# Kernel tuning notes

Hardware: AMD Instinct MI355X
Metric: run time of the kernel (lower is better)

The kernel has to match this reference:

```python
import jax, jax.numpy as jnp
import numpy as np

EPS = 1e-12

def _l2norm(x):
    return x / jnp.maximum(jnp.linalg.norm(x, axis=-1, keepdims=True), EPS)

def setup_inputs() -> dict:
    key = jax.random.key(0)
    ks = jax.random.split(key, 11)
    B, L, HID, M = 64, 512, 768, 128
    R, P, T = 64, 8, 32
    return {
        "hidden_states": jax.random.normal(ks[0], (B, L, HID), dtype=jnp.float32),
        "ctx_mask": jax.random.randint(ks[1], (B, L), 0, 2, dtype=jnp.int32),
        "between_mask": jax.random.randint(ks[2], (B, L), 0, 2, dtype=jnp.int32),
        "subj_type_id": jax.random.randint(ks[3], (B,), 0, T, dtype=jnp.int32),
        "obj_type_id": jax.random.randint(ks[4], (B,), 0, T, dtype=jnp.int32),
        "subj_first": jax.random.randint(ks[5], (B,), 0, 2, dtype=jnp.int32),
        "proj_W": jax.random.normal(ks[6], (HID, M), dtype=jnp.float32) * 0.02,
        "label_probes": jax.random.normal(ks[7], (R, P, M), dtype=jnp.float32) * 0.02,
        "subj_type_W": jax.random.normal(ks[8], (T, M), dtype=jnp.float32) * 0.02,
        "obj_type_W": jax.random.normal(ks[9], (T, M), dtype=jnp.float32) * 0.02,
        "dir_W": jax.random.normal(ks[10], (2, M), dtype=jnp.float32) * 0.02,
    }

def reference(hidden_states, ctx_mask, between_mask, subj_type_id, obj_type_id,
              subj_first, proj_W, label_probes, subj_type_W, obj_type_W, dir_W):
    # Document token embeddings: project + L2 normalize. [B, L, M]
    D = _l2norm(hidden_states @ proj_W)

    between = between_mask.astype(bool)
    ctx = ctx_mask.astype(bool)
    has_between = jnp.any(between, axis=1)  # [B]
    evidence = jnp.where(has_between[:, None], between, ctx)  # [B, L]

    # Conditioned probes: [B, R, P, M]
    Q = (label_probes[None]
         + subj_type_W[subj_type_id][:, None, None]
         + obj_type_W[obj_type_id][:, None, None]
         + dir_W[subj_first][:, None, None])
    Q = _l2norm(Q)

    # MaxSim: [B, R, P, L]
    sim = jnp.einsum('brhm,blm->brhl', Q, D)
    sim = jnp.where(evidence[:, None, None, :], sim, -10000.0)
    mx = sim.max(axis=3)                        # [B, R, P]
    mx = jnp.where(mx > -1000.0, mx, 0.0)       # zero out fully-masked probes
    logits = mx.sum(axis=2)                     # [B, R]
    return logits
```

## Files before the change

kernel.cpp:

```cpp
#include <hip/hip_runtime.h>
#include <hip/hip_bf16.h>

typedef __attribute__((ext_vector_type(8))) __bf16 bf16x8;
typedef __attribute__((ext_vector_type(4))) float f32x4;

#define B_   64
#define L_   512
#define HID_ 768
#define M_   128
#define R_   64
#define P_   8

__device__ __forceinline__ int swz(int row, int k, int stride) {
    return row * stride + (k ^ ((row & 7) << 3));
}
__device__ __forceinline__ int swz4(int row, int k) {
    return row * 128 + (k ^ ((row & 15) << 3));
}

#define GLL16(gp, lp)                                                        \
    __builtin_amdgcn_global_load_lds(                                        \
        (const __attribute__((address_space(1))) void*)(gp),                 \
        (__attribute__((address_space(3))) void*)(lp), 16, 0, 0)

__device__ __forceinline__ bf16x8 cvt8(float4 f0, float4 f1) {
    bf16x8 v;
    v[0]=(__bf16)f0.x; v[1]=(__bf16)f0.y; v[2]=(__bf16)f0.z; v[3]=(__bf16)f0.w;
    v[4]=(__bf16)f1.x; v[5]=(__bf16)f1.y; v[6]=(__bf16)f1.z; v[7]=(__bf16)f1.w;
    return v;
}

__global__ __launch_bounds__(256) void k_wt(const float* __restrict__ W,
                                            __bf16* __restrict__ Wt) {
    int idx = blockIdx.x * 256 + threadIdx.x;
    int k = idx >> 7, n = idx & 127;
    int c = k >> 6, kk = k & 63;
    Wt[c * 8192 + n * 64 + (kk ^ ((n & 7) << 3))] = (__bf16)W[idx];
}

__global__ __launch_bounds__(512, 4) void k_proj(const float* __restrict__ hidden,
                                                 const __bf16* __restrict__ Wt,
                                                 __bf16* __restrict__ D) {
    __shared__ __align__(16) float  Alf[2][64 * 64];
    __shared__ __align__(16) __bf16 Bl[2][128 * 64];
    __shared__ float nbuf[2][64];
    const int t = threadIdx.x;
    const int lane = t & 63, w = t >> 6;
    const int rlo = lane & 15, g = lane >> 4;
    const int rb = w & 3, ch = w >> 2;
    const int row0 = blockIdx.x * 512 + blockIdx.y * 64;

    f32x4 acc[4] = {};

    const int sr0 = t >> 4;
    const int scg = t & 15;
    const float* hbase = hidden + (size_t)row0 * HID_;

#define STAGE_A(ci_, buf_)                                                     \
    {                                                                          \
        _Pragma("unroll")                                                      \
        for (int h = 0; h < 2; ++h) {                                          \
            const int row = h * 32 + sr0;                                      \
            const int cgs = scg ^ (row & 7);                                   \
            GLL16(hbase + (size_t)row * HID_ + (ci_) * 64 + cgs * 4,           \
                  &Alf[buf_][(h * 8 + w) * 256 + lane * 4]);                   \
        }                                                                      \
    }
#define STAGE_B(ci_, buf_)                                                     \
    {                                                                          \
        const __bf16* wsrc = Wt + (ci_) * 8192 + w * 1024;                     \
        GLL16(wsrc + lane * 8,       &Bl[buf_][w * 1024]);                     \
        GLL16(wsrc + 512 + lane * 8, &Bl[buf_][w * 1024 + 512]);               \
    }

    STAGE_A(0, 0);
    STAGE_B(0, 0);

    for (int ci = 0; ci < 12; ++ci) {
        const int cur = ci & 1;
        if (ci < 11) {
            STAGE_A(ci + 1, cur ^ 1);
            STAGE_B(ci + 1, cur ^ 1);
            asm volatile("s_waitcnt vmcnt(4)" ::: "memory");
        } else {
            asm volatile("s_waitcnt vmcnt(0)" ::: "memory");
        }
        __builtin_amdgcn_sched_barrier(0);
        __builtin_amdgcn_s_barrier();

#pragma unroll
        for (int s = 0; s < 2; ++s) {
            const int row = rb * 16 + rlo;
            const int kkg = s * 8 + g * 2;
            const int x = row & 7;
            float4 a0 = *(const float4*)&Alf[cur][row * 64 + ((kkg ^ x) * 4)];
            float4 a1 = *(const float4*)&Alf[cur][row * 64 + (((kkg + 1) ^ x) * 4)];
            bf16x8 aF = cvt8(a0, a1);
            const int kk = s * 32 + g * 8;
#pragma unroll
            for (int c = 0; c < 4; ++c) {
                bf16x8 bF = *(const bf16x8*)&Bl[cur][swz(ch * 64 + c * 16 + rlo, kk, 64)];
                acc[c] = __builtin_amdgcn_mfma_f32_16x16x32_bf16(aF, bF, acc[c], 0, 0, 0);
            }
        }
        __builtin_amdgcn_s_barrier();
    }
#undef STAGE_A
#undef STAGE_B

    float ss[4] = {0.f, 0.f, 0.f, 0.f};
#pragma unroll
    for (int c = 0; c < 4; ++c)
#pragma unroll
        for (int r = 0; r < 4; ++r) ss[r] += acc[c][r] * acc[c][r];
#pragma unroll
    for (int r = 0; r < 4; ++r)
#pragma unroll
        for (int off = 1; off < 16; off <<= 1) ss[r] += __shfl_xor(ss[r], off);
    if (rlo == 0) {
#pragma unroll
        for (int r = 0; r < 4; ++r) nbuf[ch][rb * 16 + g * 4 + r] = ss[r];
    }
    __syncthreads();
    float sc[4];
#pragma unroll
    for (int r = 0; r < 4; ++r) {
        float tot = nbuf[0][rb * 16 + g * 4 + r] + nbuf[1][rb * 16 + g * 4 + r];
        sc[r] = 1.0f / fmaxf(sqrtf(tot), 1e-12f);
    }

    __bf16* Dst = (__bf16*)Alf;
#pragma unroll
    for (int c = 0; c < 4; ++c)
#pragma unroll
        for (int r = 0; r < 4; ++r) {
            int row = rb * 16 + g * 4 + r;
            int col = ch * 64 + c * 16 + rlo;
            Dst[swz4(row, col)] = (__bf16)(acc[c][r] * sc[r]);
        }
    __syncthreads();
#pragma unroll
    for (int h = 0; h < 2; ++h) {
        int row = (t >> 4) + h * 32;
        int seg = t & 15;
        bf16x8 v = *(const bf16x8*)&Dst[row * 128 + seg * 8];
        *(bf16x8*)(D + (size_t)(row0 + row) * M_ + seg * 8) = v;
    }
}

__global__ __launch_bounds__(256) void k_sim(const float* __restrict__ lp,
                                             const float* __restrict__ sW,
                                             const float* __restrict__ oW,
                                             const float* __restrict__ dW,
                                             const int* __restrict__ st,
                                             const int* __restrict__ ot,
                                             const int* __restrict__ sf,
                                             const int* __restrict__ ctx,
                                             const int* __restrict__ btw,
                                             const __bf16* __restrict__ D,
                                             float* __restrict__ out) {
    __shared__ __align__(16) __bf16 Dl[2][128 * 128];
    __shared__ float evl[L_];
    __shared__ int anyf;
    const int t = threadIdx.x;
    const int lane = t & 63, w = t >> 6;
    const int rlo = lane & 15, g = lane >> 4;
    const int b = blockIdx.x, pt = blockIdx.y;

    const __bf16* Db = D + (size_t)b * L_ * M_;

#pragma unroll
    for (int q = 0; q < 8; ++q)
        GLL16(Db + q * 2048 + w * 512 + lane * 8, &Dl[0][q * 2048 + w * 512]);

    if (t == 0) anyf = 0;
    __syncthreads();
    int v0 = btw[b * L_ + t], v1 = btw[b * L_ + t + 256];
    int c0 = ctx[b * L_ + t], c1 = ctx[b * L_ + t + 256];
    if (v0 | v1) anyf = 1;
    __syncthreads();
    const int any = anyf;
    evl[t]       = (any ? v0 : c0) ? 1.0f : 0.0f;
    evl[t + 256] = (any ? v1 : c1) ? 1.0f : 0.0f;

    const int sb = st[b], ob = ot[b], db = sf[b];
    const float* sv = sW + sb * M_;
    const float* ov = oW + ob * M_;
    const float* dv = dW + db * M_;
    bf16x8 qF[2][4];
#pragma unroll
    for (int pt2 = 0; pt2 < 2; ++pt2) {
        const float* lpp = lp + (size_t)(pt * 128 + w * 32 + pt2 * 16 + rlo) * M_;
        float qv[32];
        float ssq = 0.f;
#pragma unroll
        for (int ks = 0; ks < 4; ++ks) {
#pragma unroll
            for (int h = 0; h < 2; ++h) {
                const int m0 = ks * 32 + g * 8 + h * 4;
                float4 a  = *(const float4*)(lpp + m0);
                float4 s4 = *(const float4*)(sv + m0);
                float4 o4 = *(const float4*)(ov + m0);
                float4 d4 = *(const float4*)(dv + m0);
                float x0 = a.x + s4.x + o4.x + d4.x;
                float x1 = a.y + s4.y + o4.y + d4.y;
                float x2 = a.z + s4.z + o4.z + d4.z;
                float x3 = a.w + s4.w + o4.w + d4.w;
                qv[ks * 8 + h * 4 + 0] = x0;
                qv[ks * 8 + h * 4 + 1] = x1;
                qv[ks * 8 + h * 4 + 2] = x2;
                qv[ks * 8 + h * 4 + 3] = x3;
                ssq += x0 * x0 + x1 * x1 + x2 * x2 + x3 * x3;
            }
        }
        ssq += __shfl_xor(ssq, 16);
        ssq += __shfl_xor(ssq, 32);
        const float scq = 1.0f / fmaxf(sqrtf(ssq), 1e-12f);
#pragma unroll
        for (int ks = 0; ks < 4; ++ks)
#pragma unroll
            for (int j = 0; j < 8; ++j)
                qF[pt2][ks][j] = (__bf16)(qv[ks * 8 + j] * scq);
    }

    __syncthreads();

    float vmax[2][4];
#pragma unroll
    for (int pt2 = 0; pt2 < 2; ++pt2)
#pragma unroll
        for (int r = 0; r < 4; ++r) vmax[pt2][r] = -1e30f;

    for (int tc = 0; tc < 4; ++tc) {
        const int cur = tc & 1;
        if (tc < 3) {
#pragma unroll
            for (int q = 0; q < 8; ++q)
                GLL16(Db + (tc + 1) * 16384 + q * 2048 + w * 512 + lane * 8,
                      &Dl[cur ^ 1][q * 2048 + w * 512]);
        }
#pragma unroll
        for (int tt = 0; tt < 8; ++tt) {
            f32x4 pacc[2] = {};
#pragma unroll
            for (int ks = 0; ks < 4; ++ks) {
                bf16x8 bF = *(const bf16x8*)&Dl[cur][swz4(tt * 16 + rlo, ks * 32 + g * 8)];
                pacc[0] = __builtin_amdgcn_mfma_f32_16x16x32_bf16(qF[0][ks], bF, pacc[0], 0, 0, 0);
                pacc[1] = __builtin_amdgcn_mfma_f32_16x16x32_bf16(qF[1][ks], bF, pacc[1], 0, 0, 0);
            }
            const float e = evl[tc * 128 + tt * 16 + rlo];
#pragma unroll
            for (int pt2 = 0; pt2 < 2; ++pt2)
#pragma unroll
                for (int r = 0; r < 4; ++r) {
                    float sv2 = (e > 0.5f) ? pacc[pt2][r] : -1e4f;
                    vmax[pt2][r] = fmaxf(vmax[pt2][r], sv2);
                }
        }
        __syncthreads();
    }

#pragma unroll
    for (int pt2 = 0; pt2 < 2; ++pt2)
#pragma unroll
        for (int r = 0; r < 4; ++r)
#pragma unroll
            for (int off = 1; off < 16; off <<= 1)
                vmax[pt2][r] = fmaxf(vmax[pt2][r], __shfl_xor(vmax[pt2][r], off));

#pragma unroll
    for (int pt2 = 0; pt2 < 2; ++pt2) {
        float psum = 0.f;
#pragma unroll
        for (int r = 0; r < 4; ++r)
            psum += (vmax[pt2][r] > -1000.0f) ? vmax[pt2][r] : 0.0f;
        float rtot = psum + __shfl_xor(psum, 16);
        if ((lane & 31) == 0) {
            int rr = pt * 16 + w * 4 + pt2 * 2 + (g >> 1);
            out[b * R_ + rr] = rtot;
        }
    }
}

extern "C" void kernel_launch(void* const* d_in, const int* in_sizes, int n_in,
                              void* d_out, int out_size, void* d_ws, size_t ws_size,
                              hipStream_t stream) {
    const float* hidden = (const float*)d_in[0];
    const int*   ctx    = (const int*)d_in[1];
    const int*   btw    = (const int*)d_in[2];
    const int*   st     = (const int*)d_in[3];
    const int*   ot     = (const int*)d_in[4];
    const int*   sf     = (const int*)d_in[5];
    const float* W      = (const float*)d_in[6];
    const float* lp     = (const float*)d_in[7];
    const float* sW     = (const float*)d_in[8];
    const float* oW     = (const float*)d_in[9];
    const float* dW     = (const float*)d_in[10];
    float* out = (float*)d_out;

    char* ws = (char*)d_ws;
    __bf16* Wt = (__bf16*)ws;
    __bf16* D  = (__bf16*)(ws + 196608);

    k_wt  <<<(HID_ * M_) / 256, 256, 0, stream>>>(W, Wt);
    k_proj<<<dim3(B_, 8), 512, 0, stream>>>(hidden, Wt, D);
    k_sim <<<dim3(B_, 4), 256, 0, stream>>>(lp, sW, oW, dW, st, ot, sf, ctx, btw, D, out);
}
```

Baseline: 42.07 us.

## Fuse projection and MaxSim kernels with per-batch atomic flag synchronization

Merges the projection GEMM and the MaxSim kernel into one launch. Each of the 8 blocks per batch writes its 64-row D slice, then waits on a per-batch atomic counter until all 8 slices are written, and computes 8 relations itself. This removes a kernel launch boundary and overlaps probe construction with the projection. It relies on all 8 blocks of a batch being co-resident; a bounded spin with a timeout guards against deadlock but could silently read stale D if that timeout is hit.

```diff
diff --git a/kernel.cpp b/kernel.cpp
--- a/kernel.cpp
+++ b/kernel.cpp
@@ -31,27 +31,46 @@
 }
 
 __global__ __launch_bounds__(256) void k_wt(const float* __restrict__ W,
-                                            __bf16* __restrict__ Wt) {
+                                            __bf16* __restrict__ Wt,
+                                            int* __restrict__ flag) {
+    if (blockIdx.x == 0 && threadIdx.x < B_) flag[threadIdx.x] = 0;
     int idx = blockIdx.x * 256 + threadIdx.x;
     int k = idx >> 7, n = idx & 127;
     int c = k >> 6, kk = k & 63;
     Wt[c * 8192 + n * 64 + (kk ^ ((n & 7) << 3))] = (__bf16)W[idx];
 }
 
-__global__ __launch_bounds__(512, 4) void k_proj(const float* __restrict__ hidden,
-                                                 const __bf16* __restrict__ Wt,
-                                                 __bf16* __restrict__ D) {
-    __shared__ __align__(16) float  Alf[2][64 * 64];
-    __shared__ __align__(16) __bf16 Bl[2][128 * 64];
+__global__ __launch_bounds__(512, 4) void k_fused(
+        const float* __restrict__ hidden, const __bf16* __restrict__ Wt,
+        const float* __restrict__ lp, const float* __restrict__ sW,
+        const float* __restrict__ oW, const float* __restrict__ dW,
+        const int* __restrict__ st, const int* __restrict__ ot,
+        const int* __restrict__ sf, const int* __restrict__ ctx,
+        const int* __restrict__ btw, __bf16* __restrict__ D,
+        int* __restrict__ flag, float* __restrict__ out) {
+    __shared__ __align__(16) char smem[65536];
     __shared__ float nbuf[2][64];
+    __shared__ float evl[L_];
+    __shared__ float pmx[2][64];
+    __shared__ int anyf;
+    auto Alf = reinterpret_cast<float(*)[4096]>(smem);
+    auto Bl  = reinterpret_cast<__bf16(*)[8192]>(smem + 32768);
+    auto Dl  = reinterpret_cast<__bf16(*)[16384]>(smem);
+
     const int t = threadIdx.x;
     const int lane = t & 63, w = t >> 6;
     const int rlo = lane & 15, g = lane >> 4;
     const int rb = w & 3, ch = w >> 2;
-    const int row0 = blockIdx.x * 512 + blockIdx.y * 64;
+    const int b = blockIdx.x, j = blockIdx.y;
+    const int row0 = b * L_ + j * 64;
+
+    if (t == 0) anyf = 0;
+    const int bt = btw[b * L_ + t];
+    const int ct = ctx[b * L_ + t];
+    __syncthreads();
+    if (bt) anyf = 1;
 
     f32x4 acc[4] = {};
-
     const int sr0 = t >> 4;
     const int scg = t & 15;
     const float* hbase = hidden + (size_t)row0 * HID_;
@@ -87,7 +106,6 @@
         }
         __builtin_amdgcn_sched_barrier(0);
         __builtin_amdgcn_s_barrier();
-
 #pragma unroll
         for (int s = 0; s < 2; ++s) {
             const int row = rb * 16 + rlo;
@@ -129,7 +147,10 @@
         sc[r] = 1.0f / fmaxf(sqrtf(tot), 1e-12f);
     }
 
-    __bf16* Dst = (__bf16*)Alf;
+    const int any = anyf;
+    evl[t] = ((any ? bt : ct) != 0) ? 1.0f : 0.0f;
+
+    __bf16* Dst = (__bf16*)smem;
 #pragma unroll
     for (int c = 0; c < 4; ++c)
 #pragma unroll
@@ -146,51 +167,15 @@
         bf16x8 v = *(const bf16x8*)&Dst[row * 128 + seg * 8];
         *(bf16x8*)(D + (size_t)(row0 + row) * M_ + seg * 8) = v;
     }
-}
-
-__global__ __launch_bounds__(256) void k_sim(const float* __restrict__ lp,
-                                             const float* __restrict__ sW,
-                                             const float* __restrict__ oW,
-                                             const float* __restrict__ dW,
-                                             const int* __restrict__ st,
-                                             const int* __restrict__ ot,
-                                             const int* __restrict__ sf,
-                                             const int* __restrict__ ctx,
-                                             const int* __restrict__ btw,
-                                             const __bf16* __restrict__ D,
-                                             float* __restrict__ out) {
-    __shared__ __align__(16) __bf16 Dl[2][128 * 128];
-    __shared__ float evl[L_];
-    __shared__ int anyf;
-    const int t = threadIdx.x;
-    const int lane = t & 63, w = t >> 6;
-    const int rlo = lane & 15, g = lane >> 4;
-    const int b = blockIdx.x, pt = blockIdx.y;
-
-    const __bf16* Db = D + (size_t)b * L_ * M_;
-
-#pragma unroll
-    for (int q = 0; q < 8; ++q)
-        GLL16(Db + q * 2048 + w * 512 + lane * 8, &Dl[0][q * 2048 + w * 512]);
-
-    if (t == 0) anyf = 0;
-    __syncthreads();
-    int v0 = btw[b * L_ + t], v1 = btw[b * L_ + t + 256];
-    int c0 = ctx[b * L_ + t], c1 = ctx[b * L_ + t + 256];
-    if (v0 | v1) anyf = 1;
-    __syncthreads();
-    const int any = anyf;
-    evl[t]       = (any ? v0 : c0) ? 1.0f : 0.0f;
-    evl[t + 256] = (any ? v1 : c1) ? 1.0f : 0.0f;
-
+
+    const int tau = w & 3, u = w >> 2;
     const int sb = st[b], ob = ot[b], db = sf[b];
     const float* sv = sW + sb * M_;
     const float* ov = oW + ob * M_;
     const float* dv = dW + db * M_;
-    bf16x8 qF[2][4];
-#pragma unroll
-    for (int pt2 = 0; pt2 < 2; ++pt2) {
-        const float* lpp = lp + (size_t)(pt * 128 + w * 32 + pt2 * 16 + rlo) * M_;
+    bf16x8 qF[4];
+    {
+        const float* lpp = lp + (size_t)(j * 64 + tau * 16 + rlo) * M_;
         float qv[32];
         float ssq = 0.f;
 #pragma unroll
@@ -219,66 +204,78 @@
 #pragma unroll
         for (int ks = 0; ks < 4; ++ks)
 #pragma unroll
-            for (int j = 0; j < 8; ++j)
-                qF[pt2][ks][j] = (__bf16)(qv[ks * 8 + j] * scq);
-    }
-
-    __syncthreads();
-
-    float vmax[2][4];
-#pragma unroll
-    for (int pt2 = 0; pt2 < 2; ++pt2)
-#pragma unroll
-        for (int r = 0; r < 4; ++r) vmax[pt2][r] = -1e30f;
+            for (int q = 0; q < 8; ++q)
+                qF[ks][q] = (__bf16)(qv[ks * 8 + q] * scq);
+    }
+
+    __syncthreads();
+    if (t == 0) {
+        __threadfence();
+        atomicAdd(&flag[b], 1);
+        int it = 0;
+        while (atomicAdd(&flag[b], 0) < 8 && it < (1 << 17)) {
+            __builtin_amdgcn_s_sleep(8);
+            ++it;
+        }
+    }
+    __syncthreads();
+
+    const __bf16* Db = D + (size_t)b * L_ * M_;
+#pragma unroll
+    for (int q = 0; q < 4; ++q)
+        GLL16(Db + w * 2048 + q * 512 + lane * 8, &Dl[0][w * 2048 + q * 512]);
+
+    float vm[4] = {-1e30f, -1e30f, -1e30f, -1e30f};
 
     for (int tc = 0; tc < 4; ++tc) {
         const int cur = tc & 1;
         if (tc < 3) {
 #pragma unroll
-            for (int q = 0; q < 8; ++q)
-                GLL16(Db + (tc + 1) * 16384 + q * 2048 + w * 512 + lane * 8,
-                      &Dl[cur ^ 1][q * 2048 + w * 512]);
-        }
-#pragma unroll
-        for (int tt = 0; tt < 8; ++tt) {
-            f32x4 pacc[2] = {};
+            for (int q = 0; q < 4; ++q)
+                GLL16(Db + (tc + 1) * 16384 + w * 2048 + q * 512 + lane * 8,
+                      &Dl[cur ^ 1][w * 2048 + q * 512]);
+            asm volatile("s_waitcnt vmcnt(4)" ::: "memory");
+        } else {
+            asm volatile("s_waitcnt vmcnt(0)" ::: "memory");
+        }
+        __builtin_amdgcn_sched_barrier(0);
+        __builtin_amdgcn_s_barrier();
+#pragma unroll
+        for (int i = 0; i < 4; ++i) {
+            const int tt = u * 4 + i;
+            f32x4 pacc = {};
 #pragma unroll
             for (int ks = 0; ks < 4; ++ks) {
                 bf16x8 bF = *(const bf16x8*)&Dl[cur][swz4(tt * 16 + rlo, ks * 32 + g * 8)];
-                pacc[0] = __builtin_amdgcn_mfma_f32_16x16x32_bf16(qF[0][ks], bF, pacc[0], 0, 0, 0);
-                pacc[1] = __builtin_amdgcn_mfma_f32_16x16x32_bf16(qF[1][ks], bF, pacc[1], 0, 0, 0);
+                pacc = __builtin_amdgcn_mfma_f32_16x16x32_bf16(qF[ks], bF, pacc, 0, 0, 0);
             }
             const float e = evl[tc * 128 + tt * 16 + rlo];
 #pragma unroll
-            for (int pt2 = 0; pt2 < 2; ++pt2)
-#pragma unroll
-                for (int r = 0; r < 4; ++r) {
-                    float sv2 = (e > 0.5f) ? pacc[pt2][r] : -1e4f;
-                    vmax[pt2][r] = fmaxf(vmax[pt2][r], sv2);
-                }
-        }
-        __syncthreads();
-    }
-
-#pragma unroll
-    for (int pt2 = 0; pt2 < 2; ++pt2)
-#pragma unroll
-        for (int r = 0; r < 4; ++r)
-#pragma unroll
-            for (int off = 1; off < 16; off <<= 1)
-                vmax[pt2][r] = fmaxf(vmax[pt2][r], __shfl_xor(vmax[pt2][r], off));
-
-#pragma unroll
-    for (int pt2 = 0; pt2 < 2; ++pt2) {
-        float psum = 0.f;
-#pragma unroll
-        for (int r = 0; r < 4; ++r)
-            psum += (vmax[pt2][r] > -1000.0f) ? vmax[pt2][r] : 0.0f;
-        float rtot = psum + __shfl_xor(psum, 16);
-        if ((lane & 31) == 0) {
-            int rr = pt * 16 + w * 4 + pt2 * 2 + (g >> 1);
-            out[b * R_ + rr] = rtot;
-        }
+            for (int r = 0; r < 4; ++r) {
+                float sv2 = (e > 0.5f) ? pacc[r] : -1e4f;
+                vm[r] = fmaxf(vm[r], sv2);
+            }
+        }
+        __builtin_amdgcn_s_barrier();
+    }
+
+#pragma unroll
+    for (int r = 0; r < 4; ++r)
+#pragma unroll
+        for (int off = 1; off < 16; off <<= 1)
+            vm[r] = fmaxf(vm[r], __shfl_xor(vm[r], off));
+    if (rlo == 0) {
+#pragma unroll
+        for (int r = 0; r < 4; ++r) pmx[u][tau * 16 + g * 4 + r] = vm[r];
+    }
+    __syncthreads();
+    if (t < 64) {
+        float m = fmaxf(pmx[0][t], pmx[1][t]);
+        m = (m > -1000.0f) ? m : 0.0f;
+        m += __shfl_xor(m, 1);
+        m += __shfl_xor(m, 2);
+        m += __shfl_xor(m, 4);
+        if ((t & 7) == 0) out[b * R_ + j * 8 + (t >> 3)] = m;
     }
 }
 
@@ -299,10 +296,11 @@
     float* out = (float*)d_out;
 
     char* ws = (char*)d_ws;
-    __bf16* Wt = (__bf16*)ws;
-    __bf16* D  = (__bf16*)(ws + 196608);
-
-    k_wt  <<<(HID_ * M_) / 256, 256, 0, stream>>>(W, Wt);
-    k_proj<<<dim3(B_, 8), 512, 0, stream>>>(hidden, Wt, D);
-    k_sim <<<dim3(B_, 4), 256, 0, stream>>>(lp, sW, oW, dW, st, ot, sf, ctx, btw, D, out);
-}
+    __bf16* Wt   = (__bf16*)ws;
+    __bf16* D    = (__bf16*)(ws + 196608);
+    int*    flag = (int*)(ws + 196608 + 8388608);
+
+    k_wt   <<<(HID_ * M_) / 256, 256, 0, stream>>>(W, Wt, flag);
+    k_fused<<<dim3(B_, 8), 512, 0, stream>>>(hidden, Wt, lp, sW, oW, dW,
+                                             st, ot, sf, ctx, btw, D, flag, out);
+}
```

Result: slower. 58.61 us (+39.3%).
